# Performance work log

Hardware: AMD Instinct MI355X
Metric: run time of the kernel (lower is better)

## Reference

```python
import jax, jax.numpy as jnp
import numpy as np

NBINS = (128, 64, 32)
N_REGIONS = 5000
N_REGIONS_OI = 500
N_POINTS = 262144
SUM_H = sum(NBINS)            # 224
SUM_W = sum(n - 1 for n in NBINS)  # 221


def _spline_level(x, uw_region, uh_pt, local_ix):
    """One quadratic-spline level.
    x: [N] inputs in [0,1); uw_region: [R, n-1] region unnormalized widths;
    uh_pt: [N, n] per-point unnormalized heights (embedding + delta);
    local_ix: [N] int mapping points -> rows of uw_region.
    """
    # region-level widths / bin locations (calculate_widths / calculate_bin_locations)
    widths = jax.nn.softmax(uw_region, axis=-1)                # [R, n-1]
    bl = jnp.cumsum(widths, axis=-1)
    bl = bl.at[:, -1].set(1.0)
    bin_locations = jnp.pad(bl, ((0, 0), (1, 0)))              # [R, n]

    # gather per point (index_select(0, local_region_ix))
    widths_pt = widths[local_ix]                               # [N, n-1]
    bin_loc_pt = bin_locations[local_ix]                       # [N, n]

    # calculate_heights: exp then normalize so trapezoid integral == 1
    he = jnp.exp(uh_pt)                                        # [N, n]
    area = jnp.sum(0.5 * (he[:, :-1] + he[:, 1:]) * widths_pt, axis=-1, keepdims=True)
    heights = he / area                                        # [N, n]

    # calculate_bin_left_cdf
    cdf = jnp.cumsum(0.5 * (heights[:, :-1] + heights[:, 1:]) * widths_pt, axis=-1)
    cdf = cdf.at[:, -1].set(1.0)
    bin_left_cdf = jnp.pad(cdf, ((0, 0), (1, 0)))              # [N, n]

    # searchsorted(bin_locations, x, side='left') - 1, clamped to valid bins
    n = bin_loc_pt.shape[-1]
    bin_idx = jnp.clip(jnp.sum(bin_loc_pt < x[:, None], axis=-1) - 1, 0, n - 2)  # [N]

    take = lambda a, i: jnp.take_along_axis(a, i[:, None], axis=-1)[:, 0]
    in_loc = take(bin_loc_pt, bin_idx)
    in_w = take(widths_pt, bin_idx)
    in_cdf = take(bin_left_cdf, bin_idx)
    h_l = take(heights, bin_idx)
    h_r = take(heights, bin_idx + 1)

    alpha = (x - in_loc) / in_w
    a = 0.5 * (h_r - h_l) * in_w
    b = h_l * in_w
    out = a * alpha * alpha + b * alpha + in_cdf
    logabsdet = jnp.log(alpha * (h_r - h_l) + h_l)
    return out, logabsdet


def setup_inputs() -> dict:
    key = jax.random.key(0)
    k1, k2, k3, k4, k5, k6 = jax.random.split(key, 6)
    x = jax.random.uniform(k1, (N_POINTS,), dtype=jnp.float32)
    regions_oi = jax.random.randint(k2, (N_REGIONS_OI,), 0, N_REGIONS, dtype=jnp.int32)
    local_region_ix = jax.random.randint(k3, (N_POINTS,), 0, N_REGIONS_OI, dtype=jnp.int32)
    delta = jax.random.normal(k4, (N_POINTS, SUM_H), dtype=jnp.float32)
    # learned sparse embedding tables (init to random for a nontrivial baseline)
    heights_emb = 0.1 * jax.random.normal(k5, (N_REGIONS, SUM_H), dtype=jnp.float32)
    widths_emb = 0.1 * jax.random.normal(k6, (N_REGIONS, SUM_W), dtype=jnp.float32)
    return {"x": x, "regions_oi": regions_oi, "local_region_ix": local_region_ix,
            "delta": delta, "heights_emb": heights_emb, "widths_emb": widths_emb}


def reference(x, regions_oi, local_region_ix, delta, heights_emb, widths_emb):
    uh_all = heights_emb[regions_oi]   # [R, 224]
    uw_all = widths_emb[regions_oi]    # [R, 221]
    out = x
    logdet = jnp.zeros_like(x)
    oh = 0
    ow = 0
    for n in NBINS:
        uw = uw_all[:, ow:ow + (n - 1)]                               # [R, n-1]
        uh_pt = uh_all[local_region_ix][:, oh:oh + n] + delta[:, oh:oh + n]  # [N, n]
        out, ld = _spline_level(out, uw, uh_pt, local_region_ix)
        logdet = logdet + ld
        oh += n
        ow += n - 1
    return out, logdet
```

## Files before the change

### kernel.cpp

```cpp
#include <hip/hip_runtime.h>

#define NPOINTS 262144
#define SUMH 224
#define SUMW 221
#define NREG 500


__device__ __forceinline__ float rlane(float v, int l) {
  return __int_as_float(__builtin_amdgcn_readlane(__float_as_int(v), l));
}

template<int CTRL>
__device__ __forceinline__ float dpp_add(float x) {
  return x + __int_as_float(__builtin_amdgcn_update_dpp(0, __float_as_int(x), CTRL, 0xF, 0xF, false));
}
template<int CTRL>
__device__ __forceinline__ float dpp_max(float x) {
  return fmaxf(x, __int_as_float(__builtin_amdgcn_update_dpp(__float_as_int(x), __float_as_int(x), CTRL, 0xF, 0xF, false)));
}

__device__ __forceinline__ float wave_sum(float x) {
  x = dpp_add<0x111>(x);
  x = dpp_add<0x112>(x);
  x = dpp_add<0x114>(x);
  x = dpp_add<0x118>(x);
  x = dpp_add<0x142>(x);
  x = dpp_add<0x143>(x);
  return rlane(x, 63);
}
__device__ __forceinline__ float wave_max(float x) {
  x = dpp_max<0x111>(x);
  x = dpp_max<0x112>(x);
  x = dpp_max<0x114>(x);
  x = dpp_max<0x118>(x);
  x = dpp_max<0x142>(x);
  x = dpp_max<0x143>(x);
  return rlane(x, 63);
}


template<int NM1, int SRC, int DST, int NSLOT>
__device__ __forceinline__ void region_level(const float* __restrict__ wrow,
    float* __restrict__ wW, float* __restrict__ wB, int lane, float* lds)
{
  float v0 = (lane < NM1) ? wrow[SRC + lane] : -1e30f;
  float v1 = -1e30f;
  if constexpr (NSLOT == 128) {
    if (lane + 64 < NM1) v1 = wrow[SRC + lane + 64];
  }
  float m = wave_max(fmaxf(v0, v1));
  float e0 = __expf(v0 - m);
  float e1 = (NSLOT == 128) ? __expf(v1 - m) : 0.0f;
  float s = wave_sum(e0 + e1);
  float inv = 1.0f / s;
  if (lane < NSLOT) { wW[DST + lane] = 0.5f * e0 * inv; lds[lane] = e0; }
  if constexpr (NSLOT == 128) { wW[DST + lane + 64] = 0.5f * e1 * inv; lds[lane + 64] = e1; }
  __syncthreads();
  if (lane == 0) {
    wB[DST] = 0.0f;
    float run = 0.0f;
    for (int k = 0; k < NM1; ++k) {
      run += lds[k];
      wB[DST + 1 + k] = (k == NM1 - 1) ? 1.0f : run * inv;
    }
  }
  __syncthreads();
}

__global__ void __launch_bounds__(64) region_kernel(
    const int* __restrict__ roi, const float* __restrict__ wemb,
    float* __restrict__ wsW, float* __restrict__ wsB)
{
  __shared__ float lds[128];
  int rix = blockIdx.x;
  int lane = threadIdx.x;
  int greg = roi[rix];
  const float* wrow = wemb + (size_t)greg * SUMW;
  float* wW = wsW + (size_t)rix * SUMH;
  float* wB = wsB + (size_t)rix * SUMH;
  region_level<127,   0,   0, 128>(wrow, wW, wB, lane, lds);
  region_level< 63, 127, 128,  64>(wrow, wW, wB, lane, lds);
  region_level< 31, 190, 192,  32>(wrow, wW, wB, lane, lds);
}


template<int N, int OFF>
__device__ __forceinline__ void spline_level(float& xv, float& logdet,
    const float* __restrict__ U, const float* __restrict__ D,
    const float* __restrict__ Wt, const float* __restrict__ Bt, int lane)
{
  float area, part, hl, hr, inloc, inw;
  if constexpr (N == 128) {
    int k0 = lane, k1 = lane + 64;
    float bl0 = Bt[OFF + k0], bl1 = Bt[OFF + k1];
    float wh0 = Wt[OFF + k0], wh1 = Wt[OFF + k1];
    float he0 = __expf(U[OFF + k0] + D[OFF + k0]);
    float he1 = __expf(U[OFF + k1] + D[OFF + k1]);
    float hn0 = __expf(U[OFF + k0 + 1] + D[OFF + k0 + 1]);
    float hn1 = __expf(U[OFF + k1 + 1] + D[OFF + k1 + 1]);
    float t0 = (he0 + hn0) * wh0;
    float t1 = (he1 + hn1) * wh1;
    int cnt = __popcll(__ballot(bl0 < xv)) + __popcll(__ballot(bl1 < xv));
    int bi = min(max(cnt - 1, 0), N - 2);
    float p0 = (k0 < bi) ? t0 : 0.0f;
    float p1 = (k1 < bi) ? t1 : 0.0f;
    area = wave_sum(t0 + t1);
    part = wave_sum(p0 + p1);
    int bi1 = bi + 1;
    hl    = (bi  < 64) ? rlane(he0, bi)       : rlane(he1, (bi  - 64) & 63);
    hr    = (bi1 < 64) ? rlane(he0, bi1)      : rlane(he1, (bi1 - 64) & 63);
    inloc = (bi  < 64) ? rlane(bl0, bi)       : rlane(bl1, (bi  - 64) & 63);
    inw   = 2.0f * ((bi < 64) ? rlane(wh0, bi) : rlane(wh1, (bi - 64) & 63));
  } else {
    int k0 = (N == 32) ? min(lane, 31) : lane;
    float bl0 = Bt[OFF + k0];
    float wh0 = Wt[OFF + k0];
    float he0 = __expf(U[OFF + k0] + D[OFF + k0]);
    int in1 = min(OFF + k0 + 1, SUMH - 1);
    float hn0 = __expf(U[in1] + D[in1]);
    float t0 = (he0 + hn0) * wh0;
    int cnt = __popcll(__ballot(bl0 < xv));
    int bi = min(max(cnt - 1, 0), N - 2);
    float p0 = (k0 < bi) ? t0 : 0.0f;
    area = wave_sum(t0);
    part = wave_sum(p0);
    hl = rlane(he0, bi);
    hr = rlane(he0, bi + 1);
    inloc = rlane(bl0, bi);
    inw = 2.0f * rlane(wh0, bi);
  }
  float inv_area = __builtin_amdgcn_rcpf(area);
  float alpha = (xv - inloc) * __builtin_amdgcn_rcpf(inw);
  float dh = hr - hl;
  float o = ((0.5f * dh * alpha + hl) * alpha * inw + part) * inv_area;
  float v = alpha * dh + hl;
  logdet += (__log2f(v) - __log2f(area)) * 0.69314718055994531f;
  xv = o;
}

__global__ void __launch_bounds__(256) spline_kernel(
    const float* __restrict__ x, const int* __restrict__ roi,
    const int* __restrict__ lix, const float* __restrict__ delta,
    const float* __restrict__ hemb,
    const float* __restrict__ wsW, const float* __restrict__ wsB,
    float* __restrict__ out)
{
  int wid = (int)((blockIdx.x * blockDim.x + threadIdx.x) >> 6);
  int lane = (int)(threadIdx.x & 63);
  if (wid >= NPOINTS) return;
  float xv = x[wid];
  int r = lix[wid];
  int greg = roi[r];
  const float* U  = hemb  + (size_t)greg * SUMH;
  const float* D  = delta + (size_t)wid  * SUMH;
  const float* Wt = wsW   + (size_t)r    * SUMH;
  const float* Bt = wsB   + (size_t)r    * SUMH;
  float logdet = 0.0f;
  spline_level<128,   0>(xv, logdet, U, D, Wt, Bt, lane);
  spline_level< 64, 128>(xv, logdet, U, D, Wt, Bt, lane);
  spline_level< 32, 192>(xv, logdet, U, D, Wt, Bt, lane);
  if (lane == 0) {
    out[wid] = xv;
    out[NPOINTS + wid] = logdet;
  }
}


extern "C" void kernel_launch(void* const* d_in, const int* in_sizes, int n_in,
                              void* d_out, int out_size, void* d_ws, size_t ws_size,
                              hipStream_t stream) {
  const float* x     = (const float*)d_in[0];
  const int*   roi   = (const int*)  d_in[1];
  const int*   lix   = (const int*)  d_in[2];
  const float* delta = (const float*)d_in[3];
  const float* hemb  = (const float*)d_in[4];
  const float* wemb  = (const float*)d_in[5];

  float* wsW = (float*)d_ws;
  float* wsB = wsW + (size_t)NREG * SUMH;

  region_kernel<<<NREG, 64, 0, stream>>>(roi, wemb, wsW, wsB);
  spline_kernel<<<NPOINTS / 4, 256, 0, stream>>>(x, roi, lix, delta, hemb, wsW, wsB, (float*)d_out);
}
```

Measured before the change: 396.5 us.

## Process four points per wavefront with 16-lane groups and vectorized loads

Each wavefront now handles four points, with 16 lanes per point instead of 64. Each lane loads contiguous float4/float2 chunks of the embedding, delta and the precomputed region tables, and reductions run through 16-lane DPP group sums. The trapezoid area is rewritten as a per-height sum against precomputed half-widths of adjacent bins (HW, HM), which removes the shifted neighbour exp. The selected bin's values are re-fetched from memory and its exp is recomputed, which adds scattered loads and extra exps per level in exchange for many fewer idle lanes and wider memory accesses.

New measurement: 389.0 us. About the same (-1.9%).

```diff
diff --git a/kernel.cpp b/kernel.cpp
--- a/kernel.cpp
+++ b/kernel.cpp
@@ -5,11 +5,9 @@
 #define SUMW 221
 #define NREG 500
 
-
 __device__ __forceinline__ float rlane(float v, int l) {
   return __int_as_float(__builtin_amdgcn_readlane(__float_as_int(v), l));
 }
-
 template<int CTRL>
 __device__ __forceinline__ float dpp_add(float x) {
   return x + __int_as_float(__builtin_amdgcn_update_dpp(0, __float_as_int(x), CTRL, 0xF, 0xF, false));
@@ -18,50 +16,63 @@
 __device__ __forceinline__ float dpp_max(float x) {
   return fmaxf(x, __int_as_float(__builtin_amdgcn_update_dpp(__float_as_int(x), __float_as_int(x), CTRL, 0xF, 0xF, false)));
 }
-
 __device__ __forceinline__ float wave_sum(float x) {
-  x = dpp_add<0x111>(x);
-  x = dpp_add<0x112>(x);
-  x = dpp_add<0x114>(x);
-  x = dpp_add<0x118>(x);
-  x = dpp_add<0x142>(x);
-  x = dpp_add<0x143>(x);
+  x = dpp_add<0x111>(x); x = dpp_add<0x112>(x); x = dpp_add<0x114>(x);
+  x = dpp_add<0x118>(x); x = dpp_add<0x142>(x); x = dpp_add<0x143>(x);
   return rlane(x, 63);
 }
 __device__ __forceinline__ float wave_max(float x) {
-  x = dpp_max<0x111>(x);
-  x = dpp_max<0x112>(x);
-  x = dpp_max<0x114>(x);
-  x = dpp_max<0x118>(x);
-  x = dpp_max<0x142>(x);
-  x = dpp_max<0x143>(x);
+  x = dpp_max<0x111>(x); x = dpp_max<0x112>(x); x = dpp_max<0x114>(x);
+  x = dpp_max<0x118>(x); x = dpp_max<0x142>(x); x = dpp_max<0x143>(x);
   return rlane(x, 63);
 }
 
-
-template<int NM1, int SRC, int DST, int NSLOT>
+__device__ __forceinline__ float grp_sum(float x) {
+  x += __int_as_float(__builtin_amdgcn_update_dpp(0, __float_as_int(x), 0xB1,  0xF, 0xF, true));
+  x += __int_as_float(__builtin_amdgcn_update_dpp(0, __float_as_int(x), 0x4E,  0xF, 0xF, true));
+  x += __int_as_float(__builtin_amdgcn_update_dpp(0, __float_as_int(x), 0x141, 0xF, 0xF, true));
+  x += __int_as_float(__builtin_amdgcn_update_dpp(0, __float_as_int(x), 0x140, 0xF, 0xF, true));
+  return x;
+}
+__device__ __forceinline__ int grp_sum_i(int x) {
+  x += __builtin_amdgcn_update_dpp(0, x, 0xB1,  0xF, 0xF, true);
+  x += __builtin_amdgcn_update_dpp(0, x, 0x4E,  0xF, 0xF, true);
+  x += __builtin_amdgcn_update_dpp(0, x, 0x141, 0xF, 0xF, true);
+  x += __builtin_amdgcn_update_dpp(0, x, 0x140, 0xF, 0xF, true);
+  return x;
+}
+
+
+template<int M, int SRC, int DST, int NB>
 __device__ __forceinline__ void region_level(const float* __restrict__ wrow,
-    float* __restrict__ wW, float* __restrict__ wB, int lane, float* lds)
-{
-  float v0 = (lane < NM1) ? wrow[SRC + lane] : -1e30f;
+    float* __restrict__ BL, float* __restrict__ HW, float* __restrict__ HM,
+    int lane, float* lds)
+{
+  float v0 = (lane < M) ? wrow[SRC + lane] : -1e30f;
   float v1 = -1e30f;
-  if constexpr (NSLOT == 128) {
-    if (lane + 64 < NM1) v1 = wrow[SRC + lane + 64];
-  }
+  if constexpr (NB == 128) { if (lane + 64 < M) v1 = wrow[SRC + lane + 64]; }
   float m = wave_max(fmaxf(v0, v1));
   float e0 = __expf(v0 - m);
-  float e1 = (NSLOT == 128) ? __expf(v1 - m) : 0.0f;
+  float e1 = (NB == 128) ? __expf(v1 - m) : 0.0f;
   float s = wave_sum(e0 + e1);
   float inv = 1.0f / s;
-  if (lane < NSLOT) { wW[DST + lane] = 0.5f * e0 * inv; lds[lane] = e0; }
-  if constexpr (NSLOT == 128) { wW[DST + lane + 64] = 0.5f * e1 * inv; lds[lane + 64] = e1; }
+  if (lane < NB) lds[lane] = e0;
+  if constexpr (NB == 128) lds[lane + 64] = e1;
   __syncthreads();
+  if (lane < NB) {
+    HW[DST + lane] = 0.5f * e0 * inv;
+    HM[DST + lane] = (lane == 0) ? 0.0f : 0.5f * lds[lane - 1] * inv;
+  }
+  if constexpr (NB == 128) {
+    HW[DST + lane + 64] = 0.5f * e1 * inv;
+    HM[DST + lane + 64] = 0.5f * lds[lane + 63] * inv;
+  }
   if (lane == 0) {
-    wB[DST] = 0.0f;
+    BL[DST] = 0.0f;
     float run = 0.0f;
-    for (int k = 0; k < NM1; ++k) {
+    for (int k = 0; k < M; ++k) {
       run += lds[k];
-      wB[DST + 1 + k] = (k == NM1 - 1) ? 1.0f : run * inv;
+      BL[DST + 1 + k] = (k == M - 1) ? 1.0f : run * inv;
     }
   }
   __syncthreads();
@@ -69,99 +80,123 @@
 
 __global__ void __launch_bounds__(64) region_kernel(
     const int* __restrict__ roi, const float* __restrict__ wemb,
-    float* __restrict__ wsW, float* __restrict__ wsB)
+    float* __restrict__ wsBL, float* __restrict__ wsHW, float* __restrict__ wsHM)
 {
   __shared__ float lds[128];
   int rix = blockIdx.x;
   int lane = threadIdx.x;
   int greg = roi[rix];
   const float* wrow = wemb + (size_t)greg * SUMW;
-  float* wW = wsW + (size_t)rix * SUMH;
-  float* wB = wsB + (size_t)rix * SUMH;
-  region_level<127,   0,   0, 128>(wrow, wW, wB, lane, lds);
-  region_level< 63, 127, 128,  64>(wrow, wW, wB, lane, lds);
-  region_level< 31, 190, 192,  32>(wrow, wW, wB, lane, lds);
-}
-
-
-template<int N, int OFF>
-__device__ __forceinline__ void spline_level(float& xv, float& logdet,
+  float* BL = wsBL + (size_t)rix * SUMH;
+  float* HW = wsHW + (size_t)rix * SUMH;
+  float* HM = wsHM + (size_t)rix * SUMH;
+  region_level<127,   0,   0, 128>(wrow, BL, HW, HM, lane, lds);
+  region_level< 63, 127, 128,  64>(wrow, BL, HW, HM, lane, lds);
+  region_level< 31, 190, 192,  32>(wrow, BL, HW, HM, lane, lds);
+}
+
+
+template<int NB, int OFF, int C>
+__device__ __forceinline__ void level(float& xv, float& logdet,
     const float* __restrict__ U, const float* __restrict__ D,
-    const float* __restrict__ Wt, const float* __restrict__ Bt, int lane)
-{
-  float area, part, hl, hr, inloc, inw;
-  if constexpr (N == 128) {
-    int k0 = lane, k1 = lane + 64;
-    float bl0 = Bt[OFF + k0], bl1 = Bt[OFF + k1];
-    float wh0 = Wt[OFF + k0], wh1 = Wt[OFF + k1];
-    float he0 = __expf(U[OFF + k0] + D[OFF + k0]);
-    float he1 = __expf(U[OFF + k1] + D[OFF + k1]);
-    float hn0 = __expf(U[OFF + k0 + 1] + D[OFF + k0 + 1]);
-    float hn1 = __expf(U[OFF + k1 + 1] + D[OFF + k1 + 1]);
-    float t0 = (he0 + hn0) * wh0;
-    float t1 = (he1 + hn1) * wh1;
-    int cnt = __popcll(__ballot(bl0 < xv)) + __popcll(__ballot(bl1 < xv));
-    int bi = min(max(cnt - 1, 0), N - 2);
-    float p0 = (k0 < bi) ? t0 : 0.0f;
-    float p1 = (k1 < bi) ? t1 : 0.0f;
-    area = wave_sum(t0 + t1);
-    part = wave_sum(p0 + p1);
-    int bi1 = bi + 1;
-    hl    = (bi  < 64) ? rlane(he0, bi)       : rlane(he1, (bi  - 64) & 63);
-    hr    = (bi1 < 64) ? rlane(he0, bi1)      : rlane(he1, (bi1 - 64) & 63);
-    inloc = (bi  < 64) ? rlane(bl0, bi)       : rlane(bl1, (bi  - 64) & 63);
-    inw   = 2.0f * ((bi < 64) ? rlane(wh0, bi) : rlane(wh1, (bi - 64) & 63));
+    const float* __restrict__ BLt, const float* __restrict__ HWt,
+    const float* __restrict__ HMt, int s)
+{
+  float u[C], d[C], bl[C], hw[C], hm[C];
+  if constexpr (C >= 4) {
+#pragma unroll
+    for (int v = 0; v < C / 4; ++v) {
+      int c0 = OFF + (s * (C / 4) + v) * 4;
+      float4 a = *(const float4*)(U   + c0);
+      float4 b = *(const float4*)(D   + c0);
+      float4 e = *(const float4*)(BLt + c0);
+      float4 f = *(const float4*)(HWt + c0);
+      float4 g = *(const float4*)(HMt + c0);
+      u[4*v+0]=a.x; u[4*v+1]=a.y; u[4*v+2]=a.z; u[4*v+3]=a.w;
+      d[4*v+0]=b.x; d[4*v+1]=b.y; d[4*v+2]=b.z; d[4*v+3]=b.w;
+      bl[4*v+0]=e.x; bl[4*v+1]=e.y; bl[4*v+2]=e.z; bl[4*v+3]=e.w;
+      hw[4*v+0]=f.x; hw[4*v+1]=f.y; hw[4*v+2]=f.z; hw[4*v+3]=f.w;
+      hm[4*v+0]=g.x; hm[4*v+1]=g.y; hm[4*v+2]=g.z; hm[4*v+3]=g.w;
+    }
   } else {
-    int k0 = (N == 32) ? min(lane, 31) : lane;
-    float bl0 = Bt[OFF + k0];
-    float wh0 = Wt[OFF + k0];
-    float he0 = __expf(U[OFF + k0] + D[OFF + k0]);
-    int in1 = min(OFF + k0 + 1, SUMH - 1);
-    float hn0 = __expf(U[in1] + D[in1]);
-    float t0 = (he0 + hn0) * wh0;
-    int cnt = __popcll(__ballot(bl0 < xv));
-    int bi = min(max(cnt - 1, 0), N - 2);
-    float p0 = (k0 < bi) ? t0 : 0.0f;
-    area = wave_sum(t0);
-    part = wave_sum(p0);
-    hl = rlane(he0, bi);
-    hr = rlane(he0, bi + 1);
-    inloc = rlane(bl0, bi);
-    inw = 2.0f * rlane(wh0, bi);
-  }
+    int c0 = OFF + s * 2;
+    float2 a = *(const float2*)(U   + c0);
+    float2 b = *(const float2*)(D   + c0);
+    float2 e = *(const float2*)(BLt + c0);
+    float2 f = *(const float2*)(HWt + c0);
+    float2 g = *(const float2*)(HMt + c0);
+    u[0]=a.x; u[1]=a.y; d[0]=b.x; d[1]=b.y; bl[0]=e.x; bl[1]=e.y;
+    hw[0]=f.x; hw[1]=f.y; hm[0]=g.x; hm[1]=g.y;
+  }
+
+  int cnt = 0;
+  float he[C];
+#pragma unroll
+  for (int i = 0; i < C; ++i) {
+    he[i] = __expf(u[i] + d[i]);
+    cnt += (bl[i] < xv) ? 1 : 0;
+  }
+  cnt = grp_sum_i(cnt);
+  int bi = min(max(cnt - 1, 0), NB - 2);
+
+  float area = 0.0f, pr = 0.0f;
+#pragma unroll
+  for (int i = 0; i < C; ++i) {
+    float t = he[i] * (hw[i] + hm[i]);
+    area += t;
+    int j = s * C + i;
+    pr += (j <= bi) ? t : 0.0f;
+  }
+  area = grp_sum(area);
+  pr   = grp_sum(pr);
+
+  float inloc = BLt[OFF + bi];
+  float hwbi  = HWt[OFF + bi];
+  float hl = __expf(U[OFF + bi]     + D[OFF + bi]);
+  float hr = __expf(U[OFF + bi + 1] + D[OFF + bi + 1]);
+
+  float part = pr - hl * hwbi;
+  float inw = 2.0f * hwbi;
   float inv_area = __builtin_amdgcn_rcpf(area);
   float alpha = (xv - inloc) * __builtin_amdgcn_rcpf(inw);
   float dh = hr - hl;
-  float o = ((0.5f * dh * alpha + hl) * alpha * inw + part) * inv_area;
-  float v = alpha * dh + hl;
-  logdet += (__log2f(v) - __log2f(area)) * 0.69314718055994531f;
-  xv = o;
+  float outv = ((0.5f * dh * alpha + hl) * alpha * inw + part) * inv_area;
+  logdet += (__log2f(alpha * dh + hl) - __log2f(area)) * 0.69314718055994531f;
+  xv = outv;
 }
 
 __global__ void __launch_bounds__(256) spline_kernel(
     const float* __restrict__ x, const int* __restrict__ roi,
     const int* __restrict__ lix, const float* __restrict__ delta,
     const float* __restrict__ hemb,
-    const float* __restrict__ wsW, const float* __restrict__ wsB,
-    float* __restrict__ out)
-{
-  int wid = (int)((blockIdx.x * blockDim.x + threadIdx.x) >> 6);
+    const float* __restrict__ wsBL, const float* __restrict__ wsHW,
+    const float* __restrict__ wsHM, float* __restrict__ out)
+{
+  int tid  = (int)(blockIdx.x * blockDim.x + threadIdx.x);
+  int wid  = tid >> 6;
   int lane = (int)(threadIdx.x & 63);
-  if (wid >= NPOINTS) return;
-  float xv = x[wid];
-  int r = lix[wid];
+  int grp  = lane >> 4;
+  int s    = lane & 15;
+  int pid  = wid * 4 + grp;
+  if (pid >= NPOINTS) return;
+
+  float xv = x[pid];
+  int r    = lix[pid];
   int greg = roi[r];
-  const float* U  = hemb  + (size_t)greg * SUMH;
-  const float* D  = delta + (size_t)wid  * SUMH;
-  const float* Wt = wsW   + (size_t)r    * SUMH;
-  const float* Bt = wsB   + (size_t)r    * SUMH;
+  const float* U   = hemb  + (size_t)greg * SUMH;
+  const float* D   = delta + (size_t)pid  * SUMH;
+  const float* BLt = wsBL  + (size_t)r    * SUMH;
+  const float* HWt = wsHW  + (size_t)r    * SUMH;
+  const float* HMt = wsHM  + (size_t)r    * SUMH;
+
   float logdet = 0.0f;
-  spline_level<128,   0>(xv, logdet, U, D, Wt, Bt, lane);
-  spline_level< 64, 128>(xv, logdet, U, D, Wt, Bt, lane);
-  spline_level< 32, 192>(xv, logdet, U, D, Wt, Bt, lane);
-  if (lane == 0) {
-    out[wid] = xv;
-    out[NPOINTS + wid] = logdet;
+  level<128,   0, 8>(xv, logdet, U, D, BLt, HWt, HMt, s);
+  level< 64, 128, 4>(xv, logdet, U, D, BLt, HWt, HMt, s);
+  level< 32, 192, 2>(xv, logdet, U, D, BLt, HWt, HMt, s);
+
+  if (s == 0) {
+    out[pid] = xv;
+    out[NPOINTS + pid] = logdet;
   }
 }
 
@@ -176,9 +211,11 @@
   const float* hemb  = (const float*)d_in[4];
   const float* wemb  = (const float*)d_in[5];
 
-  float* wsW = (float*)d_ws;
-  float* wsB = wsW + (size_t)NREG * SUMH;
-
-  region_kernel<<<NREG, 64, 0, stream>>>(roi, wemb, wsW, wsB);
-  spline_kernel<<<NPOINTS / 4, 256, 0, stream>>>(x, roi, lix, delta, hemb, wsW, wsB, (float*)d_out);
-}
+  float* wsBL = (float*)d_ws;
+  float* wsHW = wsBL + (size_t)NREG * SUMH;
+  float* wsHM = wsHW + (size_t)NREG * SUMH;
+
+  region_kernel<<<NREG, 64, 0, stream>>>(roi, wemb, wsBL, wsHW, wsHM);
+  spline_kernel<<<NPOINTS / 16, 256, 0, stream>>>(x, roi, lix, delta, hemb,
+                                                  wsBL, wsHW, wsHM, (float*)d_out);
+}
```
